# Performance work log

Measured on AMD Instinct MI355X. Metric: run time of the kernel, lower is better.

Reference implementation:

```python
import jax, jax.numpy as jnp
import numpy as np

PADDED_NODE_ID = -1
B, N, F = 4096, 128, 64


def setup_inputs() -> dict:
    key = jax.random.key(0)
    k1, k2, k3, k4, k5, k6 = jax.random.split(key, 6)
    src_ids = jax.random.randint(k1, (B, N), 0, 1000, dtype=jnp.int64 if jax.config.jax_enable_x64 else jnp.int32)
    dst_ids = jax.random.randint(k2, (B, N), 0, 1000, dtype=src_ids.dtype)
    w1 = jax.random.normal(k3, (F, 1), dtype=jnp.float32) * 0.1
    b1 = jax.random.normal(k4, (F,), dtype=jnp.float32) * 0.1
    w2 = jax.random.normal(k5, (F, F), dtype=jnp.float32) * 0.1
    b2 = jax.random.normal(k6, (F,), dtype=jnp.float32) * 0.1
    return {"src_neighbour_nodes_ids": src_ids, "dst_neighbour_nodes_ids": dst_ids,
            "w1": w1, "b1": b1, "w2": w2, "b2": b2}


def _pairwise_count(a, b):
    # count[b, i] = #{ j : a[b, i] == b[b, j] }  -- batched histogram via equality
    eq = a[:, :, None] == b[:, None, :]  # [B, N, N] bool
    return eq.sum(axis=-1).astype(jnp.float32)


def _mlp(freq, w1, b1, w2, b2):
    # freq: [B, N, 2] -> Linear(1,F) -> ReLU -> Linear(F,F), then sum over dim 2
    h = freq[..., None] * w1[:, 0] + b1          # [B, N, 2, F]
    h = jax.nn.relu(h)
    out = jnp.einsum('bncf,gf->bncg', h, w2) + b2  # [B, N, 2, F]
    return out.sum(axis=2)                        # [B, N, F]


def reference(src_neighbour_nodes_ids, dst_neighbour_nodes_ids, w1, b1, w2, b2):
    src, dst = src_neighbour_nodes_ids, dst_neighbour_nodes_ids
    src_in_src = _pairwise_count(src, src)
    dst_in_dst = _pairwise_count(dst, dst)
    src_in_dst = _pairwise_count(src, dst)
    dst_in_src = _pairwise_count(dst, src)

    src_pad = (src == PADDED_NODE_ID)[..., None]
    dst_pad = (dst == PADDED_NODE_ID)[..., None]
    source_freq = jnp.where(src_pad, 0.0, jnp.stack([src_in_src, src_in_dst], axis=-1))  # [B,N,2]
    dst_freq = jnp.where(dst_pad, 0.0, jnp.stack([dst_in_dst, dst_in_src], axis=-1))      # [B,N,2]

    src_feat = _mlp(source_freq, w1, b1, w2, b2)
    dst_feat = _mlp(dst_freq, w1, b1, w2, b2)
    return src_feat, dst_feat
```

## Files before the change

kernel.cpp:

```cpp
#include <hip/hip_runtime.h>

#define BATCH 4096
#define NN 128
#define FF 64
#define NC 129
#define HIST 1000
#define PADDED_ID (-1)

__global__ void build_table_kernel(const float* __restrict__ w1,
                                   const float* __restrict__ b1,
                                   const float* __restrict__ w2,
                                   const float* __restrict__ b2,
                                   float* __restrict__ table) {
    int c = blockIdx.x;
    int g = threadIdx.x;
    float cf = (float)c;
    float acc = b2[g];
    #pragma unroll
    for (int f = 0; f < FF; ++f) {
        float h = cf * w1[f] + b1[f];
        h = h > 0.0f ? h : 0.0f;
        acc += h * w2[g * FF + f];
    }
    table[c * FF + g] = acc;
}

__global__ __launch_bounds__(256, 8)
void encode_kernel(const int* __restrict__ src,
                   const int* __restrict__ dst,
                   const float* __restrict__ table,
                   float* __restrict__ out) {
    __shared__ unsigned s_hist[HIST];
    __shared__ unsigned s_cnt[2 * NN];

    const int b   = blockIdx.x;
    const int tid = threadIdx.x;

    const int my = (tid < NN) ? src[b * NN + tid] : dst[b * NN + (tid - NN)];
    const unsigned inc = (tid < NN) ? 1u : 0x10000u;
    const bool valid = (my >= 0) && (my < HIST);

    #pragma unroll
    for (int i = tid; i < HIST; i += 256) s_hist[i] = 0u;
    __syncthreads();

    if (valid) atomicAdd(&s_hist[my], inc);
    __syncthreads();

    s_cnt[tid] = valid ? s_hist[my] : 0u;
    __syncthreads();

    const int g4 = tid & 15;
    const int n0 = tid >> 4;
    const float4* __restrict__ tab4 = (const float4*)table;
    float4* out_src = (float4*)out + (size_t)b * (NN * FF / 4);
    float4* out_dst = out_src + (size_t)BATCH * (NN * FF / 4);

    #pragma unroll
    for (int n = n0; n < NN; n += 16) {
        {
            const unsigned h = s_cnt[n];
            float4 v0 = tab4[(h & 0xffffu) * (FF / 4) + g4];
            float4 v1 = tab4[(h >> 16)     * (FF / 4) + g4];
            float4 r;
            r.x = v0.x + v1.x; r.y = v0.y + v1.y;
            r.z = v0.z + v1.z; r.w = v0.w + v1.w;
            out_src[n * (FF / 4) + g4] = r;
        }
        {
            const unsigned h = s_cnt[NN + n];
            float4 v0 = tab4[(h & 0xffffu) * (FF / 4) + g4];
            float4 v1 = tab4[(h >> 16)     * (FF / 4) + g4];
            float4 r;
            r.x = v0.x + v1.x; r.y = v0.y + v1.y;
            r.z = v0.z + v1.z; r.w = v0.w + v1.w;
            out_dst[n * (FF / 4) + g4] = r;
        }
    }
}

extern "C" void kernel_launch(void* const* d_in, const int* in_sizes, int n_in,
                              void* d_out, int out_size, void* d_ws, size_t ws_size,
                              hipStream_t stream) {
    const int*   src = (const int*)d_in[0];
    const int*   dst = (const int*)d_in[1];
    const float* w1  = (const float*)d_in[2];
    const float* b1  = (const float*)d_in[3];
    const float* w2  = (const float*)d_in[4];
    const float* b2  = (const float*)d_in[5];
    float* out   = (float*)d_out;
    float* table = (float*)d_ws;

    build_table_kernel<<<NC, FF, 0, stream>>>(w1, b1, w2, b2, table);
    encode_kernel<<<BATCH, 256, 0, stream>>>(src, dst, table, out);
}
```

Baseline: 273.3 us.

## Split counting and emission into separate kernels with LDS-cached small-count table

Splits the fused kernel in two. The first kernel builds the histogram and writes packed counts to workspace. The second kernel emits output rows with fully coalesced float4 stores, reading table entries for counts below 16 from a padded LDS copy and falling back to global memory for larger counts. This targets the per-element global gathers and the strided per-batch write pattern, at the cost of an extra kernel launch and a round trip of the counts through global memory.

New measurement: 276.0 us. No clear change (+1.0%).

```diff
diff --git a/kernel.cpp b/kernel.cpp
--- a/kernel.cpp
+++ b/kernel.cpp
@@ -5,7 +5,11 @@
 #define FF 64
 #define NC 129
 #define HIST 1000
-#define PADDED_ID (-1)
+#define NTAB 16
+#define TSTRIDE 68
+#define ROWS_PER_BLK 512
+#define TOTAL_ROWS (2 * BATCH * NN)
+#define CNT_WS_OFF 65536
 
 __global__ void build_table_kernel(const float* __restrict__ w1,
                                    const float* __restrict__ b1,
@@ -26,12 +30,10 @@
 }
 
 __global__ __launch_bounds__(256, 8)
-void encode_kernel(const int* __restrict__ src,
-                   const int* __restrict__ dst,
-                   const float* __restrict__ table,
-                   float* __restrict__ out) {
+void count_kernel(const int* __restrict__ src,
+                  const int* __restrict__ dst,
+                  unsigned* __restrict__ cnt) {
     __shared__ unsigned s_hist[HIST];
-    __shared__ unsigned s_cnt[2 * NN];
 
     const int b   = blockIdx.x;
     const int tid = threadIdx.x;
@@ -47,35 +49,52 @@
     if (valid) atomicAdd(&s_hist[my], inc);
     __syncthreads();
 
-    s_cnt[tid] = valid ? s_hist[my] : 0u;
+    const unsigned packed = valid ? s_hist[my] : 0u;
+    const int n = (tid < NN) ? tid : (tid - NN);
+    const int buf = (tid < NN) ? 0 : 1;
+    cnt[(size_t)buf * BATCH * NN + (size_t)b * NN + n] = packed;
+}
+
+__global__ __launch_bounds__(256, 8)
+void emit_kernel(const unsigned* __restrict__ cnt,
+                 const float* __restrict__ table,
+                 float* __restrict__ out) {
+    __shared__ float    s_tab[NTAB * TSTRIDE];
+    __shared__ unsigned s_c[ROWS_PER_BLK];
+
+    const int bb  = blockIdx.x;
+    const int tid = threadIdx.x;
+    const size_t row0 = (size_t)bb * ROWS_PER_BLK;
+
+    {
+        const int r = tid >> 4, c = tid & 15;
+        *(float4*)&s_tab[r * TSTRIDE + c * 4] = ((const float4*)table)[r * (FF / 4) + c];
+    }
+    s_c[tid]       = cnt[row0 + tid];
+    s_c[tid + 256] = cnt[row0 + tid + 256];
     __syncthreads();
 
-    const int g4 = tid & 15;
-    const int n0 = tid >> 4;
     const float4* __restrict__ tab4 = (const float4*)table;
-    float4* out_src = (float4*)out + (size_t)b * (NN * FF / 4);
-    float4* out_dst = out_src + (size_t)BATCH * (NN * FF / 4);
+    float4* __restrict__ out4 = (float4*)out + row0 * (FF / 4);
 
-    #pragma unroll
-    for (int n = n0; n < NN; n += 16) {
-        {
-            const unsigned h = s_cnt[n];
-            float4 v0 = tab4[(h & 0xffffu) * (FF / 4) + g4];
-            float4 v1 = tab4[(h >> 16)     * (FF / 4) + g4];
-            float4 r;
-            r.x = v0.x + v1.x; r.y = v0.y + v1.y;
-            r.z = v0.z + v1.z; r.w = v0.w + v1.w;
-            out_src[n * (FF / 4) + g4] = r;
+    #pragma unroll 4
+    for (int it = 0; it < (ROWS_PER_BLK * (FF / 4)) / 256; ++it) {
+        const int idx = it * 256 + tid;
+        const int row = idx >> 4;
+        const int g4  = idx & 15;
+        const unsigned h  = s_c[row];
+        const unsigned c0 = h & 0xffffu;
+        const unsigned c1 = h >> 16;
+        float4 v0 = *(const float4*)&s_tab[(c0 & (NTAB - 1)) * TSTRIDE + g4 * 4];
+        float4 v1 = *(const float4*)&s_tab[(c1 & (NTAB - 1)) * TSTRIDE + g4 * 4];
+        if (__builtin_expect((h & 0xfff0fff0u) != 0u, 0)) {
+            v0 = tab4[c0 * (FF / 4) + g4];
+            v1 = tab4[c1 * (FF / 4) + g4];
         }
-        {
-            const unsigned h = s_cnt[NN + n];
-            float4 v0 = tab4[(h & 0xffffu) * (FF / 4) + g4];
-            float4 v1 = tab4[(h >> 16)     * (FF / 4) + g4];
-            float4 r;
-            r.x = v0.x + v1.x; r.y = v0.y + v1.y;
-            r.z = v0.z + v1.z; r.w = v0.w + v1.w;
-            out_dst[n * (FF / 4) + g4] = r;
-        }
+        float4 r;
+        r.x = v0.x + v1.x; r.y = v0.y + v1.y;
+        r.z = v0.z + v1.z; r.w = v0.w + v1.w;
+        out4[idx] = r;
     }
 }
 
@@ -90,7 +109,9 @@
     const float* b2  = (const float*)d_in[5];
     float* out   = (float*)d_out;
     float* table = (float*)d_ws;
+    unsigned* cnt = (unsigned*)((char*)d_ws + CNT_WS_OFF);
 
     build_table_kernel<<<NC, FF, 0, stream>>>(w1, b1, w2, b2, table);
-    encode_kernel<<<BATCH, 256, 0, stream>>>(src, dst, table, out);
+    count_kernel<<<BATCH, 256, 0, stream>>>(src, dst, cnt);
+    emit_kernel<<<TOTAL_ROWS / ROWS_PER_BLK, 256, 0, stream>>>(cnt, table, out);
 }
```
